# Kernel tuning notes

Measured on AMD Instinct MI355X. Metric: run time of the kernel, lower is better.

## Reference

```python
import jax, jax.numpy as jnp
import numpy as np

N_HEAD = 16
TARGET_LENGTH = 64  # config.target_length; targets=None path uses this


def setup_inputs() -> dict:
    key = jax.random.key(0)
    ks = jax.random.split(key, 5)
    C = 1024
    s = 1.0 / np.sqrt(C)  # keep logits in a sane range
    return {
        "x": jax.random.normal(ks[0], (4, 2048, C), dtype=jnp.float32),
        "Wq": jax.random.normal(ks[1], (C, C), dtype=jnp.float32) * s,
        "bq": jnp.zeros((C,), dtype=jnp.float32),
        "Wk": jax.random.normal(ks[2], (C, C), dtype=jnp.float32) * s,
        "bk": jnp.zeros((C,), dtype=jnp.float32),
        "Wv": jax.random.normal(ks[3], (C, C), dtype=jnp.float32) * s,
        "bv": jnp.zeros((C,), dtype=jnp.float32),
        "Wp": jax.random.normal(ks[4], (C, C), dtype=jnp.float32) * s,
        "bp": jnp.zeros((C,), dtype=jnp.float32),
    }


def reference(x, Wq, bq, Wk, bk, Wv, bv, Wp, bp):
    # Dropout layers are identity in eval mode.
    B, T, C = x.shape
    H = N_HEAD
    D = C // H
    t = TARGET_LENGTH

    q = (x @ Wq + bq).reshape(B, T, H, D).transpose(0, 2, 1, 3)  # [B,H,T,D]
    k = (x @ Wk + bk).reshape(B, T, H, D).transpose(0, 2, 1, 3)
    v = (x @ Wv + bv).reshape(B, T, H, D).transpose(0, 2, 1, 3)

    att = jnp.einsum("bhid,bhjd->bhij", q, k) * (1.0 / np.sqrt(D))  # [B,H,T,T]

    # allowed iff causal (j <= i) OR in the 'context' prefix (j < T - t + 1)
    i = jnp.arange(T)[:, None]
    j = jnp.arange(T)[None, :]
    allowed = (j <= i) | (j < T - t + 1)  # [T,T]
    att = jnp.where(allowed[None, None], att, -jnp.inf)

    att = jax.nn.softmax(att, axis=-1)
    y = jnp.einsum("bhij,bhjd->bhid", att, v)  # [B,H,T,D]
    y = y.transpose(0, 2, 1, 3).reshape(B, T, C)
    return y @ Wp + bp
```

## Files before the change

### kernel.cpp

```cpp
#include <hip/hip_runtime.h>
#include <hip/hip_bf16.h>
#include <stdint.h>

#define Bn 4
#define Tn 2048
#define Cn 1024
#define Hn 16
#define Dn 64
#define Mn (Bn*Tn)
#define CTXn (Tn - 64 + 1)

typedef float f32x4 __attribute__((ext_vector_type(4)));
typedef float f32x16 __attribute__((ext_vector_type(16)));
typedef short bf16x8 __attribute__((ext_vector_type(8)));
typedef unsigned short u16x8 __attribute__((ext_vector_type(8)));
typedef unsigned short u16x4 __attribute__((ext_vector_type(4)));

__device__ __forceinline__ float bf2f(unsigned short u){
    union { uint32_t i; float f; } v; v.i = ((uint32_t)u) << 16; return v.f;
}
__device__ __forceinline__ unsigned short f2bf(float f){
    __hip_bfloat16 h = __float2bfloat16(f);
    union { __hip_bfloat16 h; unsigned short u; } v; v.h = h; return v.u;
}
__device__ __forceinline__ uint32_t cvtpk(float lo, float hi){
    uint32_t w;
    asm("v_cvt_pk_bf16_f32 %0, %1, %2" : "=v"(w) : "v"(lo), "v"(hi));
    return w;
}

#define GLD16(SRC, LDSDST) \
    __builtin_amdgcn_global_load_lds( \
        (const __attribute__((address_space(1))) uint32_t*)(SRC), \
        (__attribute__((address_space(3))) uint32_t*)(LDSDST), 16, 0, 0)

__global__ __launch_bounds__(256) void cast_x_kernel(const float* __restrict__ in,
                                                     unsigned short* __restrict__ out, int n8)
{
    int i = blockIdx.x * 256 + threadIdx.x;
    if (i >= n8) return;
    const f32x4* p = (const f32x4*)(in + (size_t)i * 8);
    f32x4 a = p[0], b = p[1];
    u16x8 o;
    o[0]=f2bf(a[0]); o[1]=f2bf(a[1]); o[2]=f2bf(a[2]); o[3]=f2bf(a[3]);
    o[4]=f2bf(b[0]); o[5]=f2bf(b[1]); o[6]=f2bf(b[2]); o[7]=f2bf(b[3]);
    *(u16x8*)(out + (size_t)i * 8) = o;
}

struct W4 { const float* W[4]; unsigned short* Wt[4]; };

__global__ __launch_bounds__(256) void castT_w_kernel(W4 p)
{
    __shared__ float tile[64][65];
    const float* W = p.W[blockIdx.z];
    unsigned short* Wt = p.Wt[blockIdx.z];
    int k0 = blockIdx.x * 64, n0 = blockIdx.y * 64;
    int tid = threadIdx.x;
    #pragma unroll
    for (int q = 0; q < 4; q++){
        int idx = q * 256 + tid;
        int r = idx >> 4, c4 = (idx & 15) * 4;
        f32x4 v = *(const f32x4*)&W[(size_t)(k0 + r) * Cn + n0 + c4];
        tile[r][c4+0]=v[0]; tile[r][c4+1]=v[1]; tile[r][c4+2]=v[2]; tile[r][c4+3]=v[3];
    }
    __syncthreads();
    #pragma unroll
    for (int q = 0; q < 4; q++){
        int idx = q * 256 + tid;
        int r = idx >> 4, c4 = (idx & 15) * 4;
        u16x4 o;
        o[0]=f2bf(tile[c4+0][r]); o[1]=f2bf(tile[c4+1][r]);
        o[2]=f2bf(tile[c4+2][r]); o[3]=f2bf(tile[c4+3][r]);
        *(u16x4*)&Wt[(size_t)(n0 + r) * Cn + k0 + c4] = o;
    }
}

struct G3 {
    const unsigned short* Bt[3];
    const float* bias[3];
    void* out[3];
};

template<int OUTBF, int TRANSV>
__global__ __launch_bounds__(256) void gemm_bt(const unsigned short* __restrict__ A,
                                               G3 g, int Ndim, int Kdim)
{
    const int tid = threadIdx.x;
    const int wave = tid >> 6, lane = tid & 63;
    const int z = blockIdx.z;
    const unsigned short* Bt = g.Bt[z];
    const float* bias = g.bias[z];
    const int m0 = blockIdx.x * 128;
    const int n0 = blockIdx.y * 128;
    const int wm = (wave >> 1) * 64;
    const int wn = (wave & 1) * 64;

    __shared__ unsigned short Alds[2][128 * 32];
    __shared__ unsigned short Blds[2][128 * 32];

    f32x4 acc[4][4];
    #pragma unroll
    for (int i = 0; i < 4; i++)
        #pragma unroll
        for (int j = 0; j < 4; j++)
            acc[i][j] = f32x4{0.f, 0.f, 0.f, 0.f};

    int rowS[2], colS[2];
    #pragma unroll
    for (int q = 0; q < 2; q++){
        int o = (wave * 2 + q) * 1024 + lane * 16;
        int r = o >> 6;
        int sl = (o >> 4) & 3;
        rowS[q] = r;
        colS[q] = (sl ^ ((r >> 1) & 3)) * 8;
    }

    int offA[4], offB[4];
    #pragma unroll
    for (int mt = 0; mt < 4; mt++){
        int r = wm + mt * 16 + (lane & 15);
        int sl = (lane >> 4) ^ ((r >> 1) & 3);
        offA[mt] = r * 32 + sl * 8;
    }
    #pragma unroll
    for (int nt = 0; nt < 4; nt++){
        int r = wn + nt * 16 + (lane & 15);
        int sl = (lane >> 4) ^ ((r >> 1) & 3);
        offB[nt] = r * 32 + sl * 8;
    }

    const size_t Abase = (size_t)m0 * Kdim;
    const size_t Bbase = (size_t)n0 * Kdim;

    #define GSTAGE(K0, BF) do { \
        _Pragma("unroll") \
        for (int q_ = 0; q_ < 2; q_++){ \
            GLD16(A  + Abase + (size_t)rowS[q_] * Kdim + (K0) + colS[q_], \
                  (char*)&Alds[BF][0] + (wave * 2 + q_) * 1024); \
            GLD16(Bt + Bbase + (size_t)rowS[q_] * Kdim + (K0) + colS[q_], \
                  (char*)&Blds[BF][0] + (wave * 2 + q_) * 1024); \
        } \
    } while (0)

    const int nks = Kdim >> 5;
    GSTAGE(0, 0);

    for (int ks = 0; ks < nks; ks++){
        const int cur = ks & 1;
        __syncthreads();
        if (ks + 1 < nks) GSTAGE((ks + 1) << 5, cur ^ 1);

        bf16x8 af[4], bfr[4];
        #pragma unroll
        for (int mt = 0; mt < 4; mt++) af[mt]  = *(const bf16x8*)&Alds[cur][offA[mt]];
        #pragma unroll
        for (int nt = 0; nt < 4; nt++) bfr[nt] = *(const bf16x8*)&Blds[cur][offB[nt]];
        __builtin_amdgcn_s_setprio(1);
        #pragma unroll
        for (int mt = 0; mt < 4; mt++)
            #pragma unroll
            for (int nt = 0; nt < 4; nt++)
                acc[mt][nt] = __builtin_amdgcn_mfma_f32_16x16x32_bf16(af[mt], bfr[nt], acc[mt][nt], 0, 0, 0);
        __builtin_amdgcn_s_setprio(0);
    }
    #undef GSTAGE

    float bv[4];
    #pragma unroll
    for (int nt = 0; nt < 4; nt++) bv[nt] = bias[n0 + wn + nt * 16 + (lane & 15)];

    #pragma unroll
    for (int mt = 0; mt < 4; mt++){
        #pragma unroll
        for (int nt = 0; nt < 4; nt++){
            const int row0 = m0 + wm + mt * 16 + (lane >> 4) * 4;
            const int col  = n0 + wn + nt * 16 + (lane & 15);
            if (OUTBF && TRANSV && z == 2){
                u16x4 o;
                #pragma unroll
                for (int r = 0; r < 4; r++) o[r] = f2bf(acc[mt][nt][r] + bv[nt]);
                const int bb = row0 >> 11, tt = row0 & 2047;
                *(u16x4*)&((unsigned short*)g.out[z])[((size_t)(bb * 1024 + col)) * 2048 + tt] = o;
            } else {
                #pragma unroll
                for (int r = 0; r < 4; r++){
                    float v = acc[mt][nt][r] + bv[nt];
                    if (OUTBF){
                        ((unsigned short*)g.out[z])[(size_t)(row0 + r) * Ndim + col] = f2bf(v);
                    } else {
                        ((float*)g.out[z])[(size_t)(row0 + r) * Ndim + col] = v;
                    }
                }
            }
        }
    }
}

__global__ __launch_bounds__(256, 4) void attn_kernel(const unsigned short* __restrict__ Q,
                                                      const unsigned short* __restrict__ K,
                                                      const unsigned short* __restrict__ Vt,
                                                      unsigned short* __restrict__ Y)
{
    const int tid = threadIdx.x;
    const int wave = tid >> 6, lane = tid & 63;
    const int il = lane & 31, hi = lane >> 5;
    const int bh = blockIdx.x;
    const int b = bh >> 4, h = bh & 15;
    const int i0 = blockIdx.y * 128 + wave * 32;
    const int i = i0 + il;

    __shared__ unsigned short Klds[2][64 * 64];
    __shared__ unsigned short Vlds[2][64 * 64];

    const float qs = 0.125f * 1.44269504f;
    bf16x8 qf[4];
    {
        const unsigned short* qp = Q + (size_t)(b * Tn + i) * Cn + h * 64 + hi * 8;
        #pragma unroll
        for (int ksd = 0; ksd < 4; ksd++){
            u16x8 raw = *(const u16x8*)(qp + ksd * 16);
            bf16x8 f;
            #pragma unroll
            for (int e = 0; e < 8; e++) f[e] = (short)f2bf(bf2f(raw[e]) * qs);
            qf[ksd] = f;
        }
    }

    f32x16 yacc[2];
    #pragma unroll
    for (int r = 0; r < 16; r++){ yacc[0][r] = 0.f; yacc[1][r] = 0.f; }
    float l_r = 0.f;

    int rowS[2], colS[2];
    #pragma unroll
    for (int q = 0; q < 2; q++){
        int o = (wave * 2 + q) * 1024 + lane * 16;
        int r = o >> 7;
        int sl = (o >> 4) & 7;
        rowS[q] = r;
        colS[q] = (sl ^ (r & 7)) * 8;
    }

    int offK[2][4];
    #pragma unroll
    for (int jblk = 0; jblk < 2; jblk++)
        #pragma unroll
        for (int ksd = 0; ksd < 4; ksd++){
            int r = jblk * 32 + il;
            offK[jblk][ksd] = r * 64 + (((ksd * 2 + hi) ^ (r & 7)) * 8);
        }

    const size_t kbase = (size_t)(b * Tn) * Cn + h * 64;
    const size_t vbase = (size_t)bh * 64 * Tn;

    #define STAGE(T, BF) do { \
        const int j_ = (T) * 64; \
        _Pragma("unroll") \
        for (int q_ = 0; q_ < 2; q_++){ \
            GLD16(K  + kbase + (size_t)(j_ + rowS[q_]) * Cn + colS[q_], \
                  (char*)&Klds[BF][0] + (wave * 2 + q_) * 1024); \
            GLD16(Vt + vbase + (size_t)rowS[q_] * Tn + j_ + colS[q_], \
                  (char*)&Vlds[BF][0] + (wave * 2 + q_) * 1024); \
        } \
    } while (0)

    STAGE(0, 0);

    for (int t = 0; t < 32; t++){
        const int cur = t & 1;
        __syncthreads();

        if (t < 31) STAGE(t + 1, cur ^ 1);

        const unsigned short* kl = &Klds[cur][0];
        const unsigned short* vl = &Vlds[cur][0];

        f32x16 s[2];
        __builtin_amdgcn_s_setprio(1);
        #pragma unroll
        for (int jblk = 0; jblk < 2; jblk++){
            f32x16 a;
            #pragma unroll
            for (int r = 0; r < 16; r++) a[r] = 0.f;
            #pragma unroll
            for (int ksd = 0; ksd < 4; ksd++){
                bf16x8 kf = *(const bf16x8*)&kl[offK[jblk][ksd]];
                a = __builtin_amdgcn_mfma_f32_32x32x16_bf16(kf, qf[ksd], a, 0, 0, 0);
            }
            s[jblk] = a;
        }
        __builtin_amdgcn_s_setprio(0);

        if (t == 31){
            const int j0 = 31 * 64;
            #pragma unroll
            for (int jblk = 0; jblk < 2; jblk++)
                #pragma unroll
                for (int r = 0; r < 16; r++){
                    int j = j0 + jblk * 32 + (r & 3) + 8 * (r >> 2) + 4 * hi;
                    if (j > i && j >= CTXn) s[jblk][r] = -1e30f;
                }
        }

        #pragma unroll
        for (int jblk = 0; jblk < 2; jblk++)
            #pragma unroll
            for (int r = 0; r < 16; r++){
                float p = __builtin_amdgcn_exp2f(s[jblk][r]);
                s[jblk][r] = p;
                l_r += p;
            }

        bf16x8 pa[4];
        #pragma unroll
        for (int jblk = 0; jblk < 2; jblk++){
            #pragma unroll
            for (int half = 0; half < 2; half++){
                const int base = half * 8;
                uint32_t W1 = cvtpk(s[jblk][base + 0], s[jblk][base + 1]);
                uint32_t W2 = cvtpk(s[jblk][base + 2], s[jblk][base + 3]);
                uint32_t W3 = cvtpk(s[jblk][base + 4], s[jblk][base + 5]);
                uint32_t W4 = cvtpk(s[jblk][base + 6], s[jblk][base + 7]);
                uint32_t Z1 = hi ? W1 : W3;
                uint32_t Z2 = hi ? W2 : W4;
                uint32_t X1 = (uint32_t)__shfl_xor((int)Z1, 32);
                uint32_t X2 = (uint32_t)__shfl_xor((int)Z2, 32);
                union { uint32_t w[4]; bf16x8 v; } u;
                u.w[0] = hi ? X1 : W1;
                u.w[1] = hi ? X2 : W2;
                u.w[2] = hi ? W3 : X1;
                u.w[3] = hi ? W4 : X2;
                pa[jblk * 2 + half] = u.v;
            }
        }

        __builtin_amdgcn_s_setprio(1);
        #pragma unroll
        for (int ks = 0; ks < 4; ks++)
            #pragma unroll
            for (int dblk = 0; dblk < 2; dblk++){
                bf16x8 vf = *(const bf16x8*)&vl[offK[dblk][ks]];
                yacc[dblk] = __builtin_amdgcn_mfma_f32_32x32x16_bf16(vf, pa[ks], yacc[dblk], 0, 0, 0);
            }
        __builtin_amdgcn_s_setprio(0);
    }
    #undef STAGE

    l_r += __shfl_xor(l_r, 32);
    float inv = __builtin_amdgcn_rcpf(l_r);
    const size_t ybase = (size_t)(b * Tn + i) * Cn + h * 64;
    #pragma unroll
    for (int dblk = 0; dblk < 2; dblk++){
        #pragma unroll
        for (int r = 0; r < 16; r += 2){
            int d = dblk * 32 + (r & 3) + 8 * (r >> 2) + 4 * hi;
            uint32_t w = cvtpk(yacc[dblk][r] * inv, yacc[dblk][r + 1] * inv);
            *(uint32_t*)&Y[ybase + d] = w;
        }
    }
}

extern "C" void kernel_launch(void* const* d_in, const int* in_sizes, int n_in,
                              void* d_out, int out_size, void* d_ws, size_t ws_size,
                              hipStream_t stream)
{
    const float* x  = (const float*)d_in[0];
    const float* Wq = (const float*)d_in[1];
    const float* bq = (const float*)d_in[2];
    const float* Wk = (const float*)d_in[3];
    const float* bk = (const float*)d_in[4];
    const float* Wv = (const float*)d_in[5];
    const float* bv = (const float*)d_in[6];
    const float* Wp = (const float*)d_in[7];
    const float* bp = (const float*)d_in[8];

    char* w = (char*)d_ws;
    unsigned short* xb  = (unsigned short*)(w);
    unsigned short* Wqt = (unsigned short*)(w + 16777216);
    unsigned short* Wkt = (unsigned short*)(w + 18874368);
    unsigned short* Wvt = (unsigned short*)(w + 20971520);
    unsigned short* Wpt = (unsigned short*)(w + 23068672);
    unsigned short* Qb  = (unsigned short*)(w + 25165824);
    unsigned short* Kb  = (unsigned short*)(w + 41943040);
    unsigned short* Vtb = (unsigned short*)(w + 75497472);
    unsigned short* Yb  = (unsigned short*)(w + 92274688);

    cast_x_kernel<<<(Mn * Cn / 8 + 255) / 256, 256, 0, stream>>>(x, xb, Mn * Cn / 8);

    W4 wp;
    wp.W[0] = Wq; wp.W[1] = Wk; wp.W[2] = Wv; wp.W[3] = Wp;
    wp.Wt[0] = Wqt; wp.Wt[1] = Wkt; wp.Wt[2] = Wvt; wp.Wt[3] = Wpt;
    castT_w_kernel<<<dim3(16, 16, 4), 256, 0, stream>>>(wp);

    G3 g;
    g.Bt[0] = Wqt; g.Bt[1] = Wkt; g.Bt[2] = Wvt;
    g.bias[0] = bq; g.bias[1] = bk; g.bias[2] = bv;
    g.out[0] = Qb; g.out[1] = Kb; g.out[2] = Vtb;
    gemm_bt<1, 1><<<dim3(64, 8, 3), 256, 0, stream>>>(xb, g, Cn, Cn);

    attn_kernel<<<dim3(Bn * Hn, Tn / 128), 256, 0, stream>>>(Qb, Kb, Vtb, Yb);

    G3 g2;
    g2.Bt[0] = Wpt; g2.Bt[1] = Wpt; g2.Bt[2] = Wpt;
    g2.bias[0] = bp; g2.bias[1] = bp; g2.bias[2] = bp;
    g2.out[0] = d_out; g2.out[1] = d_out; g2.out[2] = d_out;
    gemm_bt<0, 0><<<dim3(64, 8, 1), 256, 0, stream>>>(Yb, g2, Cn, Cn);
}
```

Measured before the change: 196.3 us.

## Process two query groups per wave in attention to reuse K/V fragments

After: 199.9 us. About the same (+1.8%).

```diff
diff --git a/kernel.cpp b/kernel.cpp
--- a/kernel.cpp
+++ b/kernel.cpp
@@ -23,10 +23,8 @@
     __hip_bfloat16 h = __float2bfloat16(f);
     union { __hip_bfloat16 h; unsigned short u; } v; v.h = h; return v.u;
 }
-__device__ __forceinline__ uint32_t cvtpk(float lo, float hi){
-    uint32_t w;
-    asm("v_cvt_pk_bf16_f32 %0, %1, %2" : "=v"(w) : "v"(lo), "v"(hi));
-    return w;
+__device__ __forceinline__ uint32_t pack2bf(float lo, float hi){
+    return ((uint32_t)f2bf(hi) << 16) | (uint32_t)f2bf(lo);
 }
 
 #define GLD16(SRC, LDSDST) \
@@ -196,7 +194,7 @@
     }
 }
 
-__global__ __launch_bounds__(256, 4) void attn_kernel(const unsigned short* __restrict__ Q,
+__global__ __launch_bounds__(256, 2) void attn_kernel(const unsigned short* __restrict__ Q,
                                                       const unsigned short* __restrict__ K,
                                                       const unsigned short* __restrict__ Vt,
                                                       unsigned short* __restrict__ Y)
@@ -206,30 +204,32 @@
     const int il = lane & 31, hi = lane >> 5;
     const int bh = blockIdx.x;
     const int b = bh >> 4, h = bh & 15;
-    const int i0 = blockIdx.y * 128 + wave * 32;
-    const int i = i0 + il;
+    const int i0 = blockIdx.y * 256 + wave * 64;
 
     __shared__ unsigned short Klds[2][64 * 64];
     __shared__ unsigned short Vlds[2][64 * 64];
 
     const float qs = 0.125f * 1.44269504f;
-    bf16x8 qf[4];
-    {
-        const unsigned short* qp = Q + (size_t)(b * Tn + i) * Cn + h * 64 + hi * 8;
+    bf16x8 qf[2][4];
+    #pragma unroll
+    for (int g = 0; g < 2; g++){
+        const unsigned short* qp = Q + (size_t)(b * Tn + i0 + g * 32 + il) * Cn + h * 64 + hi * 8;
         #pragma unroll
         for (int ksd = 0; ksd < 4; ksd++){
             u16x8 raw = *(const u16x8*)(qp + ksd * 16);
             bf16x8 f;
             #pragma unroll
             for (int e = 0; e < 8; e++) f[e] = (short)f2bf(bf2f(raw[e]) * qs);
-            qf[ksd] = f;
+            qf[g][ksd] = f;
         }
     }
 
-    f32x16 yacc[2];
-    #pragma unroll
-    for (int r = 0; r < 16; r++){ yacc[0][r] = 0.f; yacc[1][r] = 0.f; }
-    float l_r = 0.f;
+    f32x16 yacc[2][2];
+    #pragma unroll
+    for (int g = 0; g < 2; g++)
+        #pragma unroll
+        for (int r = 0; r < 16; r++){ yacc[g][0][r] = 0.f; yacc[g][1][r] = 0.f; }
+    float l_r[2] = {0.f, 0.f};
 
     int rowS[2], colS[2];
     #pragma unroll
@@ -275,87 +275,102 @@
         const unsigned short* kl = &Klds[cur][0];
         const unsigned short* vl = &Vlds[cur][0];
 
-        f32x16 s[2];
-        __builtin_amdgcn_s_setprio(1);
         #pragma unroll
         for (int jblk = 0; jblk < 2; jblk++){
-            f32x16 a;
-            #pragma unroll
-            for (int r = 0; r < 16; r++) a[r] = 0.f;
-            #pragma unroll
-            for (int ksd = 0; ksd < 4; ksd++){
-                bf16x8 kf = *(const bf16x8*)&kl[offK[jblk][ksd]];
-                a = __builtin_amdgcn_mfma_f32_32x32x16_bf16(kf, qf[ksd], a, 0, 0, 0);
-            }
-            s[jblk] = a;
+            bf16x8 kf[4];
+            #pragma unroll
+            for (int ksd = 0; ksd < 4; ksd++)
+                kf[ksd] = *(const bf16x8*)&kl[offK[jblk][ksd]];
+
+            f32x16 s2[2];
+            __builtin_amdgcn_s_setprio(1);
+            #pragma unroll
+            for (int g = 0; g < 2; g++){
+                f32x16 a;
+                #pragma unroll
+                for (int r = 0; r < 16; r++) a[r] = 0.f;
+                #pragma unroll
+                for (int ksd = 0; ksd < 4; ksd++)
+                    a = __builtin_amdgcn_mfma_f32_32x32x16_bf16(kf[ksd], qf[g][ksd], a, 0, 0, 0);
+                s2[g] = a;
+            }
+            __builtin_amdgcn_s_setprio(0);
+
+            if (t == 31){
+                const int j0 = 31 * 64;
+                #pragma unroll
+                for (int g = 0; g < 2; g++){
+                    const int ig = i0 + g * 32 + il;
+                    #pragma unroll
+                    for (int r = 0; r < 16; r++){
+                        int j = j0 + jblk * 32 + (r & 3) + 8 * (r >> 2) + 4 * hi;
+                        if (j > ig && j >= CTXn) s2[g][r] = -1e30f;
+                    }
+                }
+            }
+
+            #pragma unroll
+            for (int g = 0; g < 2; g++)
+                #pragma unroll
+                for (int r = 0; r < 16; r++){
+                    float p = __builtin_amdgcn_exp2f(s2[g][r]);
+                    s2[g][r] = p;
+                    l_r[g] += p;
+                }
+
+            bf16x8 pa[2][2];
+            #pragma unroll
+            for (int g = 0; g < 2; g++){
+                #pragma unroll
+                for (int half = 0; half < 2; half++){
+                    const int base = half * 8;
+                    uint32_t W1 = pack2bf(s2[g][base + 0], s2[g][base + 1]);
+                    uint32_t W2 = pack2bf(s2[g][base + 2], s2[g][base + 3]);
+                    uint32_t W3 = pack2bf(s2[g][base + 4], s2[g][base + 5]);
+                    uint32_t W4 = pack2bf(s2[g][base + 6], s2[g][base + 7]);
+                    uint32_t Z1 = hi ? W1 : W3;
+                    uint32_t Z2 = hi ? W2 : W4;
+                    uint32_t X1 = (uint32_t)__shfl_xor((int)Z1, 32);
+                    uint32_t X2 = (uint32_t)__shfl_xor((int)Z2, 32);
+                    union { uint32_t w[4]; bf16x8 v; } u;
+                    u.w[0] = hi ? X1 : W1;
+                    u.w[1] = hi ? X2 : W2;
+                    u.w[2] = hi ? W3 : X1;
+                    u.w[3] = hi ? W4 : X2;
+                    pa[g][half] = u.v;
+                }
+            }
+
+            __builtin_amdgcn_s_setprio(1);
+            #pragma unroll
+            for (int half = 0; half < 2; half++){
+                const int ksg = jblk * 2 + half;
+                #pragma unroll
+                for (int dblk = 0; dblk < 2; dblk++){
+                    bf16x8 vf = *(const bf16x8*)&vl[offK[dblk][ksg]];
+                    #pragma unroll
+                    for (int g = 0; g < 2; g++)
+                        yacc[g][dblk] = __builtin_amdgcn_mfma_f32_32x32x16_bf16(vf, pa[g][half], yacc[g][dblk], 0, 0, 0);
+                }
+            }
+            __builtin_amdgcn_s_setprio(0);
         }
-        __builtin_amdgcn_s_setprio(0);
-
-        if (t == 31){
-            const int j0 = 31 * 64;
-            #pragma unroll
-            for (int jblk = 0; jblk < 2; jblk++)
-                #pragma unroll
-                for (int r = 0; r < 16; r++){
-                    int j = j0 + jblk * 32 + (r & 3) + 8 * (r >> 2) + 4 * hi;
-                    if (j > i && j >= CTXn) s[jblk][r] = -1e30f;
-                }
-        }
-
-        #pragma unroll
-        for (int jblk = 0; jblk < 2; jblk++)
-            #pragma unroll
-            for (int r = 0; r < 16; r++){
-                float p = __builtin_amdgcn_exp2f(s[jblk][r]);
-                s[jblk][r] = p;
-                l_r += p;
-            }
-
-        bf16x8 pa[4];
-        #pragma unroll
-        for (int jblk = 0; jblk < 2; jblk++){
-            #pragma unroll
-            for (int half = 0; half < 2; half++){
-                const int base = half * 8;
-                uint32_t W1 = cvtpk(s[jblk][base + 0], s[jblk][base + 1]);
-                uint32_t W2 = cvtpk(s[jblk][base + 2], s[jblk][base + 3]);
-                uint32_t W3 = cvtpk(s[jblk][base + 4], s[jblk][base + 5]);
-                uint32_t W4 = cvtpk(s[jblk][base + 6], s[jblk][base + 7]);
-                uint32_t Z1 = hi ? W1 : W3;
-                uint32_t Z2 = hi ? W2 : W4;
-                uint32_t X1 = (uint32_t)__shfl_xor((int)Z1, 32);
-                uint32_t X2 = (uint32_t)__shfl_xor((int)Z2, 32);
-                union { uint32_t w[4]; bf16x8 v; } u;
-                u.w[0] = hi ? X1 : W1;
-                u.w[1] = hi ? X2 : W2;
-                u.w[2] = hi ? W3 : X1;
-                u.w[3] = hi ? W4 : X2;
-                pa[jblk * 2 + half] = u.v;
-            }
-        }
-
-        __builtin_amdgcn_s_setprio(1);
-        #pragma unroll
-        for (int ks = 0; ks < 4; ks++)
-            #pragma unroll
-            for (int dblk = 0; dblk < 2; dblk++){
-                bf16x8 vf = *(const bf16x8*)&vl[offK[dblk][ks]];
-                yacc[dblk] = __builtin_amdgcn_mfma_f32_32x32x16_bf16(vf, pa[ks], yacc[dblk], 0, 0, 0);
-            }
-        __builtin_amdgcn_s_setprio(0);
     }
     #undef STAGE
 
-    l_r += __shfl_xor(l_r, 32);
-    float inv = __builtin_amdgcn_rcpf(l_r);
-    const size_t ybase = (size_t)(b * Tn + i) * Cn + h * 64;
-    #pragma unroll
-    for (int dblk = 0; dblk < 2; dblk++){
-        #pragma unroll
-        for (int r = 0; r < 16; r += 2){
-            int d = dblk * 32 + (r & 3) + 8 * (r >> 2) + 4 * hi;
-            uint32_t w = cvtpk(yacc[dblk][r] * inv, yacc[dblk][r + 1] * inv);
-            *(uint32_t*)&Y[ybase + d] = w;
+    #pragma unroll
+    for (int g = 0; g < 2; g++){
+        float l = l_r[g] + __shfl_xor(l_r[g], 32);
+        float inv = __builtin_amdgcn_rcpf(l);
+        const size_t ybase = (size_t)(b * Tn + i0 + g * 32 + il) * Cn + h * 64;
+        #pragma unroll
+        for (int dblk = 0; dblk < 2; dblk++){
+            #pragma unroll
+            for (int r = 0; r < 16; r += 2){
+                int d = dblk * 32 + (r & 3) + 8 * (r >> 2) + 4 * hi;
+                uint32_t w = pack2bf(yacc[g][dblk][r] * inv, yacc[g][dblk][r + 1] * inv);
+                *(uint32_t*)&Y[ybase + d] = w;
+            }
         }
     }
 }
@@ -398,7 +413,7 @@
     g.out[0] = Qb; g.out[1] = Kb; g.out[2] = Vtb;
     gemm_bt<1, 1><<<dim3(64, 8, 3), 256, 0, stream>>>(xb, g, Cn, Cn);
 
-    attn_kernel<<<dim3(Bn * Hn, Tn / 128), 256, 0, stream>>>(Qb, Kb, Vtb, Yb);
+    attn_kernel<<<dim3(Bn * Hn, Tn / 256), 256, 0, stream>>>(Qb, Kb, Vtb, Yb);
 
     G3 g2;
     g2.Bt[0] = Wpt; g2.Bt[1] = Wpt; g2.Bt[2] = Wpt;
```
